# Kernel optimization log

Measured on AMD Instinct MI355X. Metric: run time of the kernel, lower is better.

Reference implementation:

```python
import jax, jax.numpy as jnp
import numpy as np
from math import sqrt

BATCH = 32
NUM_CLASSES = 81   # incl. background (class 0 skipped)
MAX_DET = 200      # max_output / per-class NMS candidate cap
IOU_T = 0.5        # criteria in decode_batch_with_nms_trace
CONF_T = 0.05      # score mask threshold


def make_dboxes():
    """Replicates dboxes_R34_coco([1200,1200]) -> (15130, 4) xywh, clipped to [0,1]."""
    fig = 1200
    feat = [50, 25, 13, 7, 3, 3]
    scales = [int(s * fig / 300) for s in [21, 45, 99, 153, 207, 261, 315]]
    ars = [[2], [2, 3], [2, 3], [2, 3], [2], [2]]
    boxes = []
    for idx, f in enumerate(feat):
        sk1 = scales[idx] / fig
        sk2 = scales[idx + 1] / fig
        sk3 = sqrt(sk1 * sk2)
        sizes = [(sk1, sk1), (sk3, sk3)]
        for a in ars[idx]:
            w, h = sk1 * sqrt(a), sk1 / sqrt(a)
            sizes += [(w, h), (h, w)]
        fk = fig // (fig // f)
        for (w, h) in sizes:
            for i in range(f):
                for j in range(f):
                    boxes.append(((j + 0.5) / fk, (i + 0.5) / fk, w, h))
    return np.clip(np.asarray(boxes, np.float32), 0.0, 1.0)


def setup_inputs() -> dict:
    key = jax.random.key(0)
    k1, k2 = jax.random.split(key)
    db = make_dboxes()                      # (15130, 4)
    N = db.shape[0]
    return {
        "bboxes_in": jax.random.normal(k1, (BATCH, 4, N), jnp.float32),
        "scores_in": jax.random.normal(k2, (BATCH, NUM_CLASSES, N), jnp.float32),
        "scale_xy": jnp.full((1,), 0.1, jnp.float32),
        "scale_wh": jnp.full((1,), 0.2, jnp.float32),
        "dboxes_xywh": jnp.asarray(db)[None],  # (1, N, 4)
    }


def _scale_back(bboxes_in, scores_in, scale_xy, scale_wh, dboxes_xywh):
    bb = jnp.transpose(bboxes_in, (0, 2, 1))          # (B, N, 4)
    sc = jnp.transpose(scores_in, (0, 2, 1))          # (B, N, L)
    d_xy, d_wh = dboxes_xywh[..., :2], dboxes_xywh[..., 2:]
    xy = bb[..., :2] * scale_xy * d_wh + d_xy
    wh = jnp.exp(bb[..., 2:] * scale_wh) * d_wh
    ltrb = jnp.concatenate([xy - 0.5 * wh, xy + 0.5 * wh], axis=-1)
    return ltrb, jax.nn.softmax(sc, axis=-1)


def _pairwise_iou(a, b):
    lt = jnp.maximum(a[:, None, :2], b[None, :, :2])
    rb = jnp.minimum(a[:, None, 2:], b[None, :, 2:])
    wh = jnp.clip(rb - lt, 0.0)
    inter = wh[..., 0] * wh[..., 1]
    area_a = (a[:, 2] - a[:, 0]) * (a[:, 3] - a[:, 1])
    area_b = (b[:, 2] - b[:, 0]) * (b[:, 3] - b[:, 1])
    return inter / (area_a[:, None] + area_b[None, :] - inter)


def _nms_one_class(boxes, cls_scores):
    """boxes (N,4), cls_scores (N,) -> (MAX_DET,4), (MAX_DET,) with suppressed = -1."""
    s = jnp.where(cls_scores > CONF_T, cls_scores, -1.0)   # mask score > 0.05
    top_s, idx = jax.lax.top_k(s, MAX_DET)                 # descending topk
    b = boxes[idx]
    iou = _pairwise_iou(b, b)                              # (K, K)
    valid = top_s > CONF_T

    def body(i, keep):  # greedy NMS over score-sorted candidates
        sup = (iou[i] > IOU_T) & keep[i] & (jnp.arange(MAX_DET) > i)
        return keep & ~sup

    keep = jax.lax.stop_gradient(jax.lax.fori_loop(0, MAX_DET, body, valid))
    return b, jnp.where(keep, top_s, -1.0)


def _decode(bboxes_in, scores_in, scale_xy, scale_wh, dboxes_xywh):
    boxes, probs = _scale_back(bboxes_in, scores_in, scale_xy, scale_wh, dboxes_xywh)
    cls_scores = jnp.transpose(probs[..., 1:], (0, 2, 1))   # (B, C=80, N); skip bg
    B, C = cls_scores.shape[0], cls_scores.shape[1]
    per_class = jax.vmap(_nms_one_class, in_axes=(None, 0))
    kb, ks = jax.vmap(per_class, in_axes=(0, 0))(boxes, cls_scores)  # (B,C,K,4),(B,C,K)
    labels = jnp.broadcast_to(
        jnp.arange(1, C + 1, dtype=jnp.int32)[:, None], (C, MAX_DET)).reshape(-1)
    kb = kb.reshape(B, C * MAX_DET, 4)
    ks = ks.reshape(B, C * MAX_DET)
    top_s, top_i = jax.lax.top_k(ks, MAX_DET)               # global top-200
    fb = jnp.take_along_axis(kb, top_i[..., None], axis=1)  # (B, 200, 4)
    fl = labels[top_i]                                      # (B, 200)
    valid = top_s > CONF_T
    return (fb * valid[..., None].astype(fb.dtype),
            jnp.where(valid, fl, 0),
            jnp.where(valid, top_s, 0.0))


def reference(bboxes_in, scores_in, scale_xy, scale_wh, dboxes_xywh):
    return _decode(bboxes_in, scores_in, scale_xy, scale_wh, dboxes_xywh)
```

## Files before the change

### kernel.cpp

```cpp
#include <hip/hip_runtime.h>
#include <stdint.h>

#define NPRIOR   15130
#define BATCH    32
#define NCLS     81
#define NCLS_OUT 80
#define NDET     200
#define CONF_T   0.05f
#define IOU_T    0.5f
#define CAND_CAP 1024
#define NGRP     5
#define GRP      16
#define NCNT     (BATCH * NCLS_OUT)

__global__ __launch_bounds__(256, 4) void decode_softmax_scatter(
    const float* __restrict__ bboxes,
    const float* __restrict__ scores,
    const float* __restrict__ scale_xy_p,
    const float* __restrict__ scale_wh_p,
    const float* __restrict__ dboxes,
    float* __restrict__ boxes_ltrb,
    unsigned int* __restrict__ counters,
    unsigned long long* __restrict__ cand_g)
{
    int tid = threadIdx.x;
    int b = blockIdx.y;
    int t = tid & 1;
    int n = blockIdx.x * 128 + (tid >> 1);
    if (n >= NPRIOR) return;

    if (t == 0) {
        float sx = scale_xy_p[0], sw = scale_wh_p[0];
        const float* bb = bboxes + (size_t)b * 4 * NPRIOR + n;
        float bx = bb[0];
        float by = bb[NPRIOR];
        float bw = bb[2 * NPRIOR];
        float bh = bb[3 * NPRIOR];
        float4 d = ((const float4*)dboxes)[n];
        float x = __fadd_rn(__fmul_rn(__fmul_rn(bx, sx), d.z), d.x);
        float y = __fadd_rn(__fmul_rn(__fmul_rn(by, sx), d.w), d.y);
        float w = __fmul_rn(expf(__fmul_rn(bw, sw)), d.z);
        float h = __fmul_rn(expf(__fmul_rn(bh, sw)), d.w);
        float hw = __fmul_rn(0.5f, w), hh = __fmul_rn(0.5f, h);
        float4 box;
        box.x = __fsub_rn(x, hw);
        box.y = __fsub_rn(y, hh);
        box.z = __fadd_rn(x, hw);
        box.w = __fadd_rn(y, hh);
        ((float4*)boxes_ltrb)[(size_t)b * NPRIOR + n] = box;
    }

    int cls0 = t * 41;
    const float* sc = scores + ((size_t)b * NCLS + cls0) * NPRIOR + n;
    float v[41];
    float mx = -INFINITY;
#pragma unroll
    for (int k = 0; k < 41; ++k) {
        if (k < 40 || t == 0) {
            v[k] = sc[(size_t)k * NPRIOR];
            mx = fmaxf(mx, v[k]);
        }
    }
    mx = fmaxf(mx, __shfl_xor(mx, 1));

#pragma unroll
    for (int k = 0; k < 41; ++k)
        if (k < 40 || t == 0)
            v[k] = expf(__fsub_rn(v[k], mx));

    float s = 0.f;
    if (t == 0) {
#pragma unroll
        for (int k = 0; k < 41; ++k) s = __fadd_rn(s, v[k]);
    }
    float se = __shfl_xor(s, 1);
    float total = 0.f;
    if (t == 1) {
        float acc = se;
#pragma unroll
        for (int k = 0; k < 40; ++k) acc = __fadd_rn(acc, v[k]);
        total = acc;
    }
    float tot_other = __shfl_xor(total, 1);
    float sum = (t == 1) ? total : tot_other;

    unsigned int invn = 0xFFFFFFFFu - (unsigned int)n;
    unsigned int cbase = (unsigned int)b * NCLS_OUT;
#pragma unroll
    for (int k = 0; k < 41; ++k) {
        if (k < 40 || t == 0) {
            int cls = cls0 + k;
            if (cls > 0) {
                float p = __fdiv_rn(v[k], sum);
                if (p > CONF_T) {
                    unsigned int idx = cbase + (unsigned int)(cls - 1);
                    unsigned int pos = atomicAdd(&counters[idx], 1u);
                    if (pos < CAND_CAP) {
                        cand_g[(size_t)idx * CAND_CAP + pos] =
                            ((unsigned long long)__float_as_uint(p) << 32) |
                            (unsigned long long)invn;
                    }
                }
            }
        }
    }
}

__device__ inline void bitonic_desc(unsigned long long* keys, int P, int tid) {
    int prevj = 64;
    for (int k = 2; k <= P; k <<= 1) {
        for (int j = k >> 1; j > 0; j >>= 1) {
            if (j >= 64 || prevj >= 64) __syncthreads();
            for (int i = tid; i < P; i += 256) {
                int l = i ^ j;
                if (l > i) {
                    unsigned long long a = keys[i], b = keys[l];
                    bool desc = ((i & k) == 0);
                    if (desc ? (a < b) : (a > b)) {
                        keys[i] = b;
                        keys[l] = a;
                    }
                }
            }
            prevj = j;
        }
    }
}

__global__ __launch_bounds__(256) void nms_class(
    const unsigned int* __restrict__ counters,
    const unsigned long long* __restrict__ cand_g,
    const float* __restrict__ boxes_ltrb,
    float* __restrict__ cls_scores,
    float* __restrict__ cls_boxes)
{
    __shared__ unsigned long long cand[CAND_CAP];
    __shared__ float4 sbox4[NDET];
    __shared__ float sscore[NDET];
    __shared__ unsigned long long rowm[NDET][4];
    __shared__ unsigned long long keepw[4];

    int tid = threadIdx.x;
    int b = blockIdx.y;
    int bc = b * NCLS_OUT + blockIdx.x;

    unsigned int cntu = counters[bc];
    int cnt = (cntu > CAND_CAP) ? CAND_CAP : (int)cntu;

    int P = 256;
    while (P < cnt) P <<= 1;

    for (int i = tid; i < P; i += 256)
        cand[i] = (i < cnt) ? cand_g[(size_t)bc * CAND_CAP + i] : 0ull;

    bitonic_desc(cand, P, tid);

    int m = cnt < NDET ? cnt : NDET;
    if (tid < m) {
        unsigned long long key = cand[tid];
        unsigned int n = 0xFFFFFFFFu - (unsigned int)(key & 0xFFFFFFFFull);
        sscore[tid] = __uint_as_float((unsigned int)(key >> 32));
        sbox4[tid] = ((const float4*)boxes_ltrb)[(size_t)b * NPRIOR + n];
    }
    __syncthreads();

    if (tid < m) {
        float4 bi = sbox4[tid];
        float area0 = __fmul_rn(__fsub_rn(bi.z, bi.x), __fsub_rn(bi.w, bi.y));
        unsigned long long w0 = 0, w1 = 0, w2 = 0, w3 = 0;
        for (int j = tid + 1; j < m; ++j) {
            float4 bj = sbox4[j];
            float ltx = fmaxf(bi.x, bj.x), lty = fmaxf(bi.y, bj.y);
            float rbx = fminf(bi.z, bj.z), rby = fminf(bi.w, bj.w);
            float iw = fmaxf(__fsub_rn(rbx, ltx), 0.f);
            float ih = fmaxf(__fsub_rn(rby, lty), 0.f);
            float inter = __fmul_rn(iw, ih);
            float areaj = __fmul_rn(__fsub_rn(bj.z, bj.x), __fsub_rn(bj.w, bj.y));
            float den = __fsub_rn(__fadd_rn(area0, areaj), inter);
            float iou = __fdiv_rn(inter, den);
            if (iou > IOU_T) {
                if (j < 64) w0 |= 1ull << j;
                else if (j < 128) w1 |= 1ull << (j - 64);
                else if (j < 192) w2 |= 1ull << (j - 128);
                else w3 |= 1ull << (j - 192);
            }
        }
        rowm[tid][0] = w0;
        rowm[tid][1] = w1;
        rowm[tid][2] = w2;
        rowm[tid][3] = w3;
    }
    __syncthreads();

    if (tid < 64) {
        int lane = tid;
        unsigned long long kreg = 0ull;
        if (lane < 4) {
            int rem = m - lane * 64;
            kreg = (rem >= 64) ? ~0ull : (rem <= 0 ? 0ull : ((1ull << rem) - 1ull));
        }
        unsigned long long cur = (lane < 4 && m > 0) ? rowm[0][lane] : 0ull;
        for (int i = 0; i < m; ++i) {
            unsigned long long nxt = (lane < 4 && (i + 1) < m) ? rowm[i + 1][lane] : 0ull;
            unsigned long long kw = __shfl(kreg, i >> 6);
            if ((kw >> (i & 63)) & 1ull) {
                if (lane < 4) kreg &= ~cur;
            }
            cur = nxt;
        }
        if (lane < 4) keepw[lane] = kreg;
    }
    __syncthreads();

    if (tid < NDET) {
        float s = -1.0f;
        if (tid < m && ((keepw[tid >> 6] >> (tid & 63)) & 1ull)) s = sscore[tid];
        cls_scores[(size_t)bc * NDET + tid] = s;
        if (tid < m)
            ((float4*)cls_boxes)[(size_t)bc * NDET + tid] = sbox4[tid];
    }
}

__global__ __launch_bounds__(256) void topk_group(
    const float* __restrict__ cls_scores,
    unsigned long long* __restrict__ grp_keys)
{
    __shared__ unsigned long long keys[4096];
    __shared__ unsigned int cnt_s;

    int tid = threadIdx.x;
    int g = blockIdx.x, b = blockIdx.y;
    if (tid == 0) cnt_s = 0;
    __syncthreads();

    int base_e = g * GRP * NDET;
    const float* sp = cls_scores + (size_t)b * NCLS_OUT * NDET + base_e;
    for (int i = tid; i < GRP * NDET; i += 256) {
        float s = sp[i];
        if (s > CONF_T) {
            unsigned int pos = atomicAdd(&cnt_s, 1u);
            unsigned int e = (unsigned int)(base_e + i);
            keys[pos] = ((unsigned long long)__float_as_uint(s) << 32) |
                        (unsigned long long)(0xFFFFFFFFu - e);
        }
    }
    __syncthreads();
    int cnt = (int)cnt_s;
    int P = 256;
    while (P < cnt) P <<= 1;
    for (int i = tid; i < P; i += 256)
        if (i >= cnt) keys[i] = 0ull;

    bitonic_desc(keys, P, tid);

    if (tid < NDET)
        grp_keys[((size_t)b * NGRP + g) * NDET + tid] = (tid < cnt) ? keys[tid] : 0ull;
}

__global__ __launch_bounds__(256) void final_topk(
    const unsigned long long* __restrict__ grp_keys,
    const float* __restrict__ cls_boxes,
    float* __restrict__ out)
{
    __shared__ unsigned long long keys[1024];
    __shared__ unsigned int cnt_s;

    int tid = threadIdx.x, b = blockIdx.x;
    if (tid == 0) cnt_s = 0;
    __syncthreads();

    for (int i = tid; i < NGRP * NDET; i += 256) {
        unsigned long long k = grp_keys[(size_t)b * NGRP * NDET + i];
        if (k != 0ull) keys[atomicAdd(&cnt_s, 1u)] = k;
    }
    __syncthreads();
    int cnt = (int)cnt_s;
    int P = 256;
    while (P < cnt) P <<= 1;
    for (int i = tid; i < P; i += 256)
        if (i >= cnt) keys[i] = 0ull;

    bitonic_desc(keys, P, tid);

    if (tid < NDET) {
        float4 bx = make_float4(0.f, 0.f, 0.f, 0.f);
        float lab = 0.f, sc = 0.f;
        if (tid < cnt) {
            unsigned long long k = keys[tid];
            unsigned int e = 0xFFFFFFFFu - (unsigned int)(k & 0xFFFFFFFFull);
            sc = __uint_as_float((unsigned int)(k >> 32));
            unsigned int c0 = e / NDET;
            bx = ((const float4*)cls_boxes)[(size_t)b * NCLS_OUT * NDET + e];
            lab = (float)(c0 + 1);
        }
        float* fb = out;
        float* fl = out + (size_t)BATCH * NDET * 4;
        float* fs = fl + (size_t)BATCH * NDET;
        ((float4*)fb)[b * NDET + tid] = bx;
        fl[b * NDET + tid] = lab;
        fs[b * NDET + tid] = sc;
    }
}

extern "C" void kernel_launch(void* const* d_in, const int* in_sizes, int n_in,
                              void* d_out, int out_size, void* d_ws, size_t ws_size,
                              hipStream_t stream) {
    const float* bboxes = (const float*)d_in[0];
    const float* scores = (const float*)d_in[1];
    const float* sxy    = (const float*)d_in[2];
    const float* swh    = (const float*)d_in[3];
    const float* dbx    = (const float*)d_in[4];
    float* out = (float*)d_out;

    char* ws = (char*)d_ws;
    size_t off = 0;
    auto alloc = [&](size_t bytes) -> char* {
        char* p = ws + off;
        off += (bytes + 255) & ~(size_t)255;
        return p;
    };
    float* boxes_ltrb            = (float*)alloc((size_t)BATCH * NPRIOR * 4 * 4);
    unsigned int* counters       = (unsigned int*)alloc((size_t)NCNT * 4);
    unsigned long long* cand_g   = (unsigned long long*)alloc((size_t)NCNT * CAND_CAP * 8);
    float* cls_scores            = (float*)alloc((size_t)BATCH * NCLS_OUT * NDET * 4);
    float* cls_boxes             = (float*)alloc((size_t)BATCH * NCLS_OUT * NDET * 4 * 4);
    unsigned long long* grp_keys = (unsigned long long*)alloc((size_t)BATCH * NGRP * NDET * 8);

    hipMemsetAsync(counters, 0, (size_t)NCNT * 4, stream);

    dim3 gridA((NPRIOR + 127) / 128, BATCH);
    decode_softmax_scatter<<<gridA, 256, 0, stream>>>(
        bboxes, scores, sxy, swh, dbx, boxes_ltrb, counters, cand_g);

    dim3 gridB(NCLS_OUT, BATCH);
    nms_class<<<gridB, 256, 0, stream>>>(counters, cand_g, boxes_ltrb, cls_scores, cls_boxes);

    dim3 gridC1(NGRP, BATCH);
    topk_group<<<gridC1, 256, 0, stream>>>(cls_scores, grp_keys);

    final_topk<<<BATCH, 256, 0, stream>>>(grp_keys, cls_boxes, out);
}
```

Before: 997.4 us.

## Use one thread per prior with three-pass streaming softmax instead of register arrays

```diff
diff --git a/kernel.cpp b/kernel.cpp
--- a/kernel.cpp
+++ b/kernel.cpp
@@ -13,7 +13,7 @@
 #define GRP      16
 #define NCNT     (BATCH * NCLS_OUT)
 
-__global__ __launch_bounds__(256, 4) void decode_softmax_scatter(
+__global__ __launch_bounds__(256) void decode_softmax_scatter(
     const float* __restrict__ bboxes,
     const float* __restrict__ scores,
     const float* __restrict__ scale_xy_p,
@@ -21,86 +21,58 @@
     const float* __restrict__ dboxes,
     float* __restrict__ boxes_ltrb,
     unsigned int* __restrict__ counters,
-    unsigned long long* __restrict__ cand_g)
+    unsigned long long* __restrict__ cand_g,
+    int z)
 {
-    int tid = threadIdx.x;
     int b = blockIdx.y;
-    int t = tid & 1;
-    int n = blockIdx.x * 128 + (tid >> 1);
+    int n = blockIdx.x * 256 + threadIdx.x;
     if (n >= NPRIOR) return;
 
-    if (t == 0) {
-        float sx = scale_xy_p[0], sw = scale_wh_p[0];
-        const float* bb = bboxes + (size_t)b * 4 * NPRIOR + n;
-        float bx = bb[0];
-        float by = bb[NPRIOR];
-        float bw = bb[2 * NPRIOR];
-        float bh = bb[3 * NPRIOR];
-        float4 d = ((const float4*)dboxes)[n];
-        float x = __fadd_rn(__fmul_rn(__fmul_rn(bx, sx), d.z), d.x);
-        float y = __fadd_rn(__fmul_rn(__fmul_rn(by, sx), d.w), d.y);
-        float w = __fmul_rn(expf(__fmul_rn(bw, sw)), d.z);
-        float h = __fmul_rn(expf(__fmul_rn(bh, sw)), d.w);
-        float hw = __fmul_rn(0.5f, w), hh = __fmul_rn(0.5f, h);
-        float4 box;
-        box.x = __fsub_rn(x, hw);
-        box.y = __fsub_rn(y, hh);
-        box.z = __fadd_rn(x, hw);
-        box.w = __fadd_rn(y, hh);
-        ((float4*)boxes_ltrb)[(size_t)b * NPRIOR + n] = box;
-    }
-
-    int cls0 = t * 41;
-    const float* sc = scores + ((size_t)b * NCLS + cls0) * NPRIOR + n;
-    float v[41];
+    float sx = scale_xy_p[0], sw = scale_wh_p[0];
+    const float* bb = bboxes + (size_t)b * 4 * NPRIOR + n;
+    float bx = bb[0];
+    float by = bb[NPRIOR];
+    float bw = bb[2 * NPRIOR];
+    float bh = bb[3 * NPRIOR];
+    float4 d = ((const float4*)dboxes)[n];
+    float x = __fadd_rn(__fmul_rn(__fmul_rn(bx, sx), d.z), d.x);
+    float y = __fadd_rn(__fmul_rn(__fmul_rn(by, sx), d.w), d.y);
+    float w = __fmul_rn(expf(__fmul_rn(bw, sw)), d.z);
+    float h = __fmul_rn(expf(__fmul_rn(bh, sw)), d.w);
+    float hw = __fmul_rn(0.5f, w), hh = __fmul_rn(0.5f, h);
+    float4 box;
+    box.x = __fsub_rn(x, hw);
+    box.y = __fsub_rn(y, hh);
+    box.z = __fadd_rn(x, hw);
+    box.w = __fadd_rn(y, hh);
+    ((float4*)boxes_ltrb)[(size_t)b * NPRIOR + n] = box;
+
+    const float* sc = scores + (size_t)b * NCLS * NPRIOR + n;
+
     float mx = -INFINITY;
 #pragma unroll
-    for (int k = 0; k < 41; ++k) {
-        if (k < 40 || t == 0) {
-            v[k] = sc[(size_t)k * NPRIOR];
-            mx = fmaxf(mx, v[k]);
-        }
-    }
-    mx = fmaxf(mx, __shfl_xor(mx, 1));
-
+    for (int c = 0; c < NCLS; ++c)
+        mx = fmaxf(mx, sc[(size_t)c * NPRIOR]);
+
+    const float* sc2 = sc + z;
+    float sum = 0.f;
 #pragma unroll
-    for (int k = 0; k < 41; ++k)
-        if (k < 40 || t == 0)
-            v[k] = expf(__fsub_rn(v[k], mx));
-
-    float s = 0.f;
-    if (t == 0) {
-#pragma unroll
-        for (int k = 0; k < 41; ++k) s = __fadd_rn(s, v[k]);
-    }
-    float se = __shfl_xor(s, 1);
-    float total = 0.f;
-    if (t == 1) {
-        float acc = se;
-#pragma unroll
-        for (int k = 0; k < 40; ++k) acc = __fadd_rn(acc, v[k]);
-        total = acc;
-    }
-    float tot_other = __shfl_xor(total, 1);
-    float sum = (t == 1) ? total : tot_other;
-
+    for (int c = 0; c < NCLS; ++c)
+        sum = __fadd_rn(sum, expf(__fsub_rn(sc2[(size_t)c * NPRIOR], mx)));
+
+    const float* sc3 = sc + 2 * z;
     unsigned int invn = 0xFFFFFFFFu - (unsigned int)n;
     unsigned int cbase = (unsigned int)b * NCLS_OUT;
 #pragma unroll
-    for (int k = 0; k < 41; ++k) {
-        if (k < 40 || t == 0) {
-            int cls = cls0 + k;
-            if (cls > 0) {
-                float p = __fdiv_rn(v[k], sum);
-                if (p > CONF_T) {
-                    unsigned int idx = cbase + (unsigned int)(cls - 1);
-                    unsigned int pos = atomicAdd(&counters[idx], 1u);
-                    if (pos < CAND_CAP) {
-                        cand_g[(size_t)idx * CAND_CAP + pos] =
-                            ((unsigned long long)__float_as_uint(p) << 32) |
-                            (unsigned long long)invn;
-                    }
-                }
+    for (int c = 1; c < NCLS; ++c) {
+        float p = __fdiv_rn(expf(__fsub_rn(sc3[(size_t)c * NPRIOR], mx)), sum);
+        if (p > CONF_T) {
+            unsigned int idx = cbase + (unsigned int)(c - 1);
+            unsigned int pos = atomicAdd(&counters[idx], 1u);
+            if (pos < CAND_CAP) {
+                cand_g[(size_t)idx * CAND_CAP + pos] =
+                    ((unsigned long long)__float_as_uint(p) << 32) |
+                    (unsigned long long)invn;
             }
         }
     }
@@ -328,9 +300,9 @@
 
     hipMemsetAsync(counters, 0, (size_t)NCNT * 4, stream);
 
-    dim3 gridA((NPRIOR + 127) / 128, BATCH);
+    dim3 gridA((NPRIOR + 255) / 256, BATCH);
     decode_softmax_scatter<<<gridA, 256, 0, stream>>>(
-        bboxes, scores, sxy, swh, dbx, boxes_ltrb, counters, cand_g);
+        bboxes, scores, sxy, swh, dbx, boxes_ltrb, counters, cand_g, 0);
 
     dim3 gridB(NCLS_OUT, BATCH);
     nms_class<<<gridB, 256, 0, stream>>>(counters, cand_g, boxes_ltrb, cls_scores, cls_boxes);
```

Result: faster. 847.9 us (-15.0%).
